# Performance work log

Measured on AMD Instinct MI355X. Metric: run time of the kernel, lower is better.

Reference implementation:

```python
import jax, jax.numpy as jnp
import numpy as np
from jax import lax

N_WIN = 232
T = 8            # timesteps
CHUNK = N_WIN // T  # 29
BETA = 0.9
THR = 1.0
POOL_DIV = 4.0 * 4.0 * 4.0  # avgpool3d kernel volume


@jax.custom_vjp
def spike(x):
    # Heaviside forward (snntorch fire: mem_shift > 0)
    return (x > 0).astype(x.dtype)

def _spike_fwd(x):
    return spike(x), x

def _spike_bwd(x, g):
    # snntorch ATan surrogate, alpha=2: grad = 1 / (1 + (pi*x)^2)
    return (g / (1.0 + (jnp.pi * x) ** 2),)

spike.defvjp(_spike_fwd, _spike_bwd)


def lif(cur, mem, beta, thr):
    # snntorch Leaky, reset_mechanism='subtract': reset uses previous mem
    reset = spike(mem - thr)
    mem_new = beta * mem + cur - reset * thr
    spk = spike(mem_new - thr)
    return spk, mem_new


def setup_inputs() -> dict:
    key = jax.random.key(0)
    ks = jax.random.split(key, 8)
    B, C, H, W = 16, 3, 96, 96
    h0, h1 = 2048, 1024
    input_dim = 47 * 47       # 2209
    in_feat = C * h1 * 13     # 39936
    return {
        "x": jax.random.normal(ks[0], (B, C, N_WIN, H, W), jnp.float32),
        "W_in": jax.random.normal(ks[1], (h0, input_dim), jnp.float32) / np.sqrt(input_dim).astype(np.float32),
        "b_in": jax.random.normal(ks[2], (h0,), jnp.float32) * 0.01,
        "W_hid": jax.random.normal(ks[3], (h1, h0), jnp.float32) / np.sqrt(h0).astype(np.float32),
        "b_hid": jax.random.normal(ks[4], (h1,), jnp.float32) * 0.01,
        "W_out": jax.random.normal(ks[5], (4, in_feat), jnp.float32) / np.sqrt(in_feat).astype(np.float32),
        "b_out": jax.random.normal(ks[6], (4,), jnp.float32) * 0.01,
    }


def reference(x, W_in, b_in, W_hid, b_hid, W_out, b_out):
    B, C, _, H, W = x.shape
    # split time into T chunks of CHUNK, pool each chunk independently
    x6 = x[:, :, : T * CHUNK].reshape(B, C, T, CHUNK, H, W)
    pooled = lax.reduce_window(x6, 0.0, lax.add,
                               (1, 1, 1, 4, 4, 4), (1, 1, 1, 2, 2, 2), "VALID") / POOL_DIV
    Dp, Hp, Wp = pooled.shape[3], pooled.shape[4], pooled.shape[5]  # 13, 47, 47
    # [T, B, C*Dp, Hp*Wp]
    xs = pooled.transpose(2, 0, 1, 3, 4, 5).reshape(T, B, C * Dp, Hp * Wp)
    # fc_in is per-step independent -> precompute for all steps
    cur_in_all = jnp.einsum("tbnf,hf->tbnh", xs, W_in) + b_in

    def step(carry, cur_in):
        m_in, m_hid, m_out = carry
        spk_in, m_in = lif(cur_in, m_in, BETA, THR)
        cur_hid = jnp.einsum("bnh,gh->bng", spk_in, W_hid) + b_hid
        spk_hid, m_hid = lif(cur_hid, m_hid, BETA, THR)
        cur_out = spk_hid.reshape(B, -1) @ W_out.T + b_out
        spk_out, m_out = lif(cur_out, m_out, BETA, 1.0)  # li_out threshold=1.0
        return (m_in, m_hid, m_out), spk_out

    init = (jnp.zeros((B, C * Dp, W_in.shape[0]), x.dtype),
            jnp.zeros((B, C * Dp, W_hid.shape[0]), x.dtype),
            jnp.zeros((B, W_out.shape[0]), x.dtype))
    _, spk_rec = lax.scan(step, init, cur_in_all)
    return spk_rec  # [T, B, n_classes]
```

## Files before the change

### kernel.cpp

```cpp
#include <hip/hip_runtime.h>
#include <hip/hip_bf16.h>

typedef unsigned short ushort_t;
typedef __bf16 bf16x8 __attribute__((ext_vector_type(8)));
typedef float f32x4 __attribute__((ext_vector_type(4)));

#define NROWS 4992
#define KPAD 2240
#define KREAL 2209
#define NH 2048

#define OFF_XS      ((size_t)0)
#define OFF_WINB    ((size_t)22364160)
#define OFF_CURIN   ((size_t)31539200)
#define OFF_CNT1    ((size_t)72433664)
#define OFF_BITS1   ((size_t)72453632)
#define OFF_CNT2    ((size_t)73731584)
#define OFF_BITS2   ((size_t)73732096)
#define ZERO_BYTES  ((size_t)(74371072 - 72433664))
#define OFF_LIST1   ((size_t)74371072)
#define OFF_LIST2   ((size_t)75649024)

__global__ __launch_bounds__(256) void convert_win(const float* __restrict__ W,
                                                   __hip_bfloat16* __restrict__ Wb) {
    int idx = blockIdx.x * 256 + threadIdx.x;
    int n = idx / KPAD, k = idx - n * KPAD;
    float v = (k < KREAL) ? W[(size_t)n * KREAL + k] : 0.f;
    Wb[idx] = __float2bfloat16(v);
}

__global__ __launch_bounds__(256) void pool_kernel(const float* __restrict__ x,
                                                   __hip_bfloat16* __restrict__ xs) {
    __shared__ float slice[9216];
    __shared__ float acc[2][2209];
    const int tid = threadIdx.x;
    const int blk = blockIdx.x;
    const int t = blk & 7;
    const int bc = blk >> 3;
    const int b = bc / 3, c = bc - b * 3;
    const float* xbase = x + ((size_t)bc * 232 + (size_t)t * 29) * 9216;

    for (int o = tid; o < 2209; o += 256) { acc[0][o] = 0.f; acc[1][o] = 0.f; }

    for (int z = 0; z < 28; ++z) {
        __syncthreads();
        const float4* src = (const float4*)(xbase + (size_t)z * 9216);
        float4* dst = (float4*)slice;
#pragma unroll
        for (int kk = 0; kk < 9; ++kk) dst[tid + kk * 256] = src[tid + kk * 256];
        __syncthreads();

        const int dmin = (z >= 3) ? ((z - 2) >> 1) : 0;
        int dmax = z >> 1; if (dmax > 12) dmax = 12;
        const bool emit = (z >= 3) && (z & 1);
        const int dem = (z - 3) >> 1;
        const int row = t * 624 + b * 39 + c * 13 + dem;

        for (int o = tid; o < 2209; o += 256) {
            int i = o / 47, j = o - i * 47;
            const float* p = slice + (2 * i) * 96 + 2 * j;
            float s = 0.f;
#pragma unroll
            for (int dy = 0; dy < 4; ++dy)
                s += p[dy * 96 + 0] + p[dy * 96 + 1] + p[dy * 96 + 2] + p[dy * 96 + 3];
            for (int d = dmin; d <= dmax; ++d) acc[d & 1][o] += s;
            if (emit) {
                int slot = dem & 1;
                xs[(size_t)row * KPAD + o] = __float2bfloat16(acc[slot][o] * 0.015625f);
                acc[slot][o] = 0.f;
            }
        }
        if (emit) {
            for (int o = KREAL + tid; o < KPAD; o += 256)
                xs[(size_t)row * KPAD + o] = __float2bfloat16(0.f);
        }
    }
}

__global__ __launch_bounds__(256) void gemm_kernel(const ushort_t* __restrict__ A,
                                                   const ushort_t* __restrict__ B,
                                                   float* __restrict__ C) {
    __shared__ ushort_t As[64 * 40];
    __shared__ ushort_t Bs[64 * 40];
    const int tid = threadIdx.x;
    const int m0 = blockIdx.y * 64, n0 = blockIdx.x * 64;
    const int lane = tid & 63, w = tid >> 6;
    const int wm = (w >> 1) * 32, wn = (w & 1) * 32;
    const int lr = lane & 15, quad = lane >> 4;

    f32x4 acc00 = {0.f,0.f,0.f,0.f}, acc01 = {0.f,0.f,0.f,0.f};
    f32x4 acc10 = {0.f,0.f,0.f,0.f}, acc11 = {0.f,0.f,0.f,0.f};

    const int r = tid >> 2, c8 = (tid & 3) * 8;
    const ushort_t* Ag = A + (size_t)(m0 + r) * KPAD + c8;
    const ushort_t* Bg = B + (size_t)(n0 + r) * KPAD + c8;
    ushort_t* Asw = &As[r * 40 + c8];
    ushort_t* Bsw = &Bs[r * 40 + c8];
    const ushort_t* Ar0 = &As[(wm + lr) * 40 + quad * 8];
    const ushort_t* Ar1 = &As[(wm + 16 + lr) * 40 + quad * 8];
    const ushort_t* Br0 = &Bs[(wn + lr) * 40 + quad * 8];
    const ushort_t* Br1 = &Bs[(wn + 16 + lr) * 40 + quad * 8];

    for (int k0 = 0; k0 < KPAD; k0 += 32) {
        __syncthreads();
        *(uint4*)Asw = *(const uint4*)(Ag + k0);
        *(uint4*)Bsw = *(const uint4*)(Bg + k0);
        __syncthreads();
        bf16x8 a0 = *(const bf16x8*)Ar0;
        bf16x8 a1 = *(const bf16x8*)Ar1;
        bf16x8 b0 = *(const bf16x8*)Br0;
        bf16x8 b1 = *(const bf16x8*)Br1;
        acc00 = __builtin_amdgcn_mfma_f32_16x16x32_bf16(a0, b0, acc00, 0, 0, 0);
        acc01 = __builtin_amdgcn_mfma_f32_16x16x32_bf16(a0, b1, acc01, 0, 0, 0);
        acc10 = __builtin_amdgcn_mfma_f32_16x16x32_bf16(a1, b0, acc10, 0, 0, 0);
        acc11 = __builtin_amdgcn_mfma_f32_16x16x32_bf16(a1, b1, acc11, 0, 0, 0);
    }
    const int colb = n0 + wn + lr;
    const int rowb = m0 + wm + quad * 4;
#pragma unroll
    for (int reg = 0; reg < 4; ++reg) {
        C[(size_t)(rowb + reg) * NH + colb]           = acc00[reg];
        C[(size_t)(rowb + reg) * NH + colb + 16]      = acc01[reg];
        C[(size_t)(rowb + 16 + reg) * NH + colb]      = acc10[reg];
        C[(size_t)(rowb + 16 + reg) * NH + colb + 16] = acc11[reg];
    }
}

__global__ __launch_bounds__(256) void lif1_kernel(const float* __restrict__ cur_in,
                                                   const float* __restrict__ b_in,
                                                   int* __restrict__ cnt1,
                                                   int* __restrict__ list1,
                                                   unsigned int* __restrict__ bits1) {
    const int h = blockIdx.x * 256 + threadIdx.x;
    const int row2 = blockIdx.y;
    const float bias = b_in[h];
    float m = 0.f;
#pragma unroll
    for (int t = 0; t < 8; ++t) {
        const int r = t * 624 + row2;
        float cur = cur_in[(size_t)r * NH + h] + bias;
        float reset = (m > 1.f) ? 1.f : 0.f;
        m = 0.9f * m + cur - reset;
        if (m > 1.f) {
            int idx = atomicAdd(&cnt1[r], 1);
            if (idx < 64) list1[r * 64 + idx] = h;
            atomicOr(&bits1[r * 64 + (h >> 5)], 1u << (h & 31));
        }
    }
}

__global__ __launch_bounds__(256) void lif2_kernel(const float* __restrict__ W_hid,
                                                   const float* __restrict__ b_hid,
                                                   const int* __restrict__ cnt1,
                                                   const int* __restrict__ list1,
                                                   const unsigned int* __restrict__ bits1,
                                                   int* __restrict__ cnt2,
                                                   int* __restrict__ list2,
                                                   unsigned int* __restrict__ bits2) {
    const int g = blockIdx.x * 256 + threadIdx.x;
    const int row2 = blockIdx.y;
    const int b = row2 / 39, n = row2 - b * 39;
    const float* Wg = W_hid + (size_t)g * NH;
    const float bias = b_hid[g];
    float m = 0.f;
    for (int t = 0; t < 8; ++t) {
        const int r = t * 624 + row2;
        float cur = bias;
        int c = cnt1[r];
        if (c > 0) {
            if (c <= 64) {
                for (int i2 = 0; i2 < c; ++i2) cur += Wg[list1[r * 64 + i2]];
            } else {
                for (int w2 = 0; w2 < 64; ++w2) {
                    unsigned int v = bits1[r * 64 + w2];
                    while (v) { int h = w2 * 32 + __ffs(v) - 1; v &= v - 1; cur += Wg[h]; }
                }
            }
        }
        float reset = (m > 1.f) ? 1.f : 0.f;
        m = 0.9f * m + cur - reset;
        if (m > 1.f) {
            int rb = t * 16 + b;
            int fidx = n * 1024 + g;
            int idx = atomicAdd(&cnt2[rb], 1);
            if (idx < 256) list2[rb * 256 + idx] = fidx;
            atomicOr(&bits2[rb * 1248 + (fidx >> 5)], 1u << (fidx & 31));
        }
    }
}

__global__ void lif3_kernel(const float* __restrict__ W_out,
                            const float* __restrict__ b_out,
                            const int* __restrict__ cnt2,
                            const int* __restrict__ list2,
                            const unsigned int* __restrict__ bits2,
                            float* __restrict__ out) {
    const int tid = threadIdx.x;
    const int b = tid >> 2, o = tid & 3;
    const float* Wo = W_out + (size_t)o * 39936;
    const float bias = b_out[o];
    float m = 0.f;
    for (int t = 0; t < 8; ++t) {
        const int rb = t * 16 + b;
        float cur = bias;
        int c = cnt2[rb];
        if (c > 0) {
            if (c <= 256) {
                for (int i2 = 0; i2 < c; ++i2) cur += Wo[list2[rb * 256 + i2]];
            } else {
                for (int w2 = 0; w2 < 1248; ++w2) {
                    unsigned int v = bits2[rb * 1248 + w2];
                    while (v) { int f = w2 * 32 + __ffs(v) - 1; v &= v - 1; cur += Wo[f]; }
                }
            }
        }
        float reset = (m > 1.f) ? 1.f : 0.f;
        m = 0.9f * m + cur - reset;
        out[t * 64 + b * 4 + o] = (m > 1.f) ? 1.f : 0.f;
    }
}

extern "C" void kernel_launch(void* const* d_in, const int* in_sizes, int n_in,
                              void* d_out, int out_size, void* d_ws, size_t ws_size,
                              hipStream_t stream) {
    const float* x     = (const float*)d_in[0];
    const float* W_in  = (const float*)d_in[1];
    const float* b_in  = (const float*)d_in[2];
    const float* W_hid = (const float*)d_in[3];
    const float* b_hid = (const float*)d_in[4];
    const float* W_out = (const float*)d_in[5];
    const float* b_out = (const float*)d_in[6];
    float* out = (float*)d_out;
    char* ws = (char*)d_ws;

    __hip_bfloat16* xs_bf  = (__hip_bfloat16*)(ws + OFF_XS);
    __hip_bfloat16* winb   = (__hip_bfloat16*)(ws + OFF_WINB);
    float*          cur_in = (float*)(ws + OFF_CURIN);
    int*            cnt1   = (int*)(ws + OFF_CNT1);
    unsigned int*   bits1  = (unsigned int*)(ws + OFF_BITS1);
    int*            cnt2   = (int*)(ws + OFF_CNT2);
    unsigned int*   bits2  = (unsigned int*)(ws + OFF_BITS2);
    int*            list1  = (int*)(ws + OFF_LIST1);
    int*            list2  = (int*)(ws + OFF_LIST2);

    hipMemsetAsync(ws + OFF_CNT1, 0, ZERO_BYTES, stream);

    convert_win<<<(2048 * KPAD) / 256, 256, 0, stream>>>(W_in, winb);
    pool_kernel<<<384, 256, 0, stream>>>(x, xs_bf);
    gemm_kernel<<<dim3(2048 / 64, NROWS / 64), 256, 0, stream>>>(
        (const ushort_t*)xs_bf, (const ushort_t*)winb, cur_in);
    lif1_kernel<<<dim3(8, 624), 256, 0, stream>>>(cur_in, b_in, cnt1, list1, bits1);
    lif2_kernel<<<dim3(4, 624), 256, 0, stream>>>(W_hid, b_hid, cnt1, list1, bits1,
                                                  cnt2, list2, bits2);
    lif3_kernel<<<1, 64, 0, stream>>>(W_out, b_out, cnt2, list2, bits2, out);
}
```

Measured before the change: 704.1 us.

## Split pooling into row bands and enlarge GEMM tiles with direct-to-LDS loads

The pooling kernel is split into four spatial row bands per (batch, channel, timestep) block. This quadruples the grid and shrinks shared memory, which should raise occupancy on the bandwidth-bound input read. The fc_in GEMM moves from 64x64 to 128x128 block tiles with a 4x4 MFMA grid per wave, which gives more operand reuse per LDS load. It also fills shared memory with global_load_lds and drops the register staging. The unpadded 32-element LDS rows may cause bank conflicts on fragment reads, and the larger accumulator array raises register pressure.

```diff
diff --git a/kernel.cpp b/kernel.cpp
--- a/kernel.cpp
+++ b/kernel.cpp
@@ -21,6 +21,10 @@
 #define OFF_LIST1   ((size_t)74371072)
 #define OFF_LIST2   ((size_t)75649024)
 
+#define GLOAD16(g, l) __builtin_amdgcn_global_load_lds( \
+    (const __attribute__((address_space(1))) void*)(g), \
+    (__attribute__((address_space(3))) void*)(l), 16, 0, 0)
+
 __global__ __launch_bounds__(256) void convert_win(const float* __restrict__ W,
                                                    __hip_bfloat16* __restrict__ Wb) {
     int idx = blockIdx.x * 256 + threadIdx.x;
@@ -31,23 +35,27 @@
 
 __global__ __launch_bounds__(256) void pool_kernel(const float* __restrict__ x,
                                                    __hip_bfloat16* __restrict__ xs) {
-    __shared__ float slice[9216];
-    __shared__ float acc[2][2209];
+    __shared__ float slice[26 * 96];
+    __shared__ float acc[2][12 * 47];
     const int tid = threadIdx.x;
+    const int band = blockIdx.y;
     const int blk = blockIdx.x;
     const int t = blk & 7;
     const int bc = blk >> 3;
     const int b = bc / 3, c = bc - b * 3;
-    const float* xbase = x + ((size_t)bc * 232 + (size_t)t * 29) * 9216;
-
-    for (int o = tid; o < 2209; o += 256) { acc[0][o] = 0.f; acc[1][o] = 0.f; }
+    const int i0 = band * 12;
+    const int ni = (band == 3) ? 11 : 12;
+    const int nyf4 = (2 * ni + 2) * 24;
+    const int nout = ni * 47;
+    const float* xbase = x + ((size_t)bc * 232 + (size_t)t * 29) * 9216 + i0 * 192;
+
+    for (int o = tid; o < nout; o += 256) { acc[0][o] = 0.f; acc[1][o] = 0.f; }
 
     for (int z = 0; z < 28; ++z) {
         __syncthreads();
         const float4* src = (const float4*)(xbase + (size_t)z * 9216);
         float4* dst = (float4*)slice;
-#pragma unroll
-        for (int kk = 0; kk < 9; ++kk) dst[tid + kk * 256] = src[tid + kk * 256];
+        for (int idx = tid; idx < nyf4; idx += 256) dst[idx] = src[idx];
         __syncthreads();
 
         const int dmin = (z >= 3) ? ((z - 2) >> 1) : 0;
@@ -56,9 +64,9 @@
         const int dem = (z - 3) >> 1;
         const int row = t * 624 + b * 39 + c * 13 + dem;
 
-        for (int o = tid; o < 2209; o += 256) {
-            int i = o / 47, j = o - i * 47;
-            const float* p = slice + (2 * i) * 96 + 2 * j;
+        for (int o = tid; o < nout; o += 256) {
+            int il = o / 47, j = o - il * 47;
+            const float* p = slice + (2 * il) * 96 + 2 * j;
             float s = 0.f;
 #pragma unroll
             for (int dy = 0; dy < 4; ++dy)
@@ -66,63 +74,73 @@
             for (int d = dmin; d <= dmax; ++d) acc[d & 1][o] += s;
             if (emit) {
                 int slot = dem & 1;
-                xs[(size_t)row * KPAD + o] = __float2bfloat16(acc[slot][o] * 0.015625f);
+                xs[(size_t)row * KPAD + i0 * 47 + o] = __float2bfloat16(acc[slot][o] * 0.015625f);
                 acc[slot][o] = 0.f;
             }
         }
-        if (emit) {
-            for (int o = KREAL + tid; o < KPAD; o += 256)
-                xs[(size_t)row * KPAD + o] = __float2bfloat16(0.f);
-        }
-    }
-}
-
+        if (emit && band == 0 && tid < KPAD - KREAL) {
+            xs[(size_t)row * KPAD + KREAL + tid] = __float2bfloat16(0.f);
+        }
+    }
+}
+
+#define BM 128
+#define BN 128
+#define BK 32
 __global__ __launch_bounds__(256) void gemm_kernel(const ushort_t* __restrict__ A,
                                                    const ushort_t* __restrict__ B,
                                                    float* __restrict__ C) {
-    __shared__ ushort_t As[64 * 40];
-    __shared__ ushort_t Bs[64 * 40];
+    __shared__ ushort_t As[BM * BK];
+    __shared__ ushort_t Bs[BN * BK];
     const int tid = threadIdx.x;
-    const int m0 = blockIdx.y * 64, n0 = blockIdx.x * 64;
+    const int m0 = blockIdx.y * BM, n0 = blockIdx.x * BN;
     const int lane = tid & 63, w = tid >> 6;
-    const int wm = (w >> 1) * 32, wn = (w & 1) * 32;
+    const int wm = (w >> 1) * 64, wn = (w & 1) * 64;
     const int lr = lane & 15, quad = lane >> 4;
 
-    f32x4 acc00 = {0.f,0.f,0.f,0.f}, acc01 = {0.f,0.f,0.f,0.f};
-    f32x4 acc10 = {0.f,0.f,0.f,0.f}, acc11 = {0.f,0.f,0.f,0.f};
-
-    const int r = tid >> 2, c8 = (tid & 3) * 8;
-    const ushort_t* Ag = A + (size_t)(m0 + r) * KPAD + c8;
-    const ushort_t* Bg = B + (size_t)(n0 + r) * KPAD + c8;
-    ushort_t* Asw = &As[r * 40 + c8];
-    ushort_t* Bsw = &Bs[r * 40 + c8];
-    const ushort_t* Ar0 = &As[(wm + lr) * 40 + quad * 8];
-    const ushort_t* Ar1 = &As[(wm + 16 + lr) * 40 + quad * 8];
-    const ushort_t* Br0 = &Bs[(wn + lr) * 40 + quad * 8];
-    const ushort_t* Br1 = &Bs[(wn + 16 + lr) * 40 + quad * 8];
-
-    for (int k0 = 0; k0 < KPAD; k0 += 32) {
-        __syncthreads();
-        *(uint4*)Asw = *(const uint4*)(Ag + k0);
-        *(uint4*)Bsw = *(const uint4*)(Bg + k0);
-        __syncthreads();
-        bf16x8 a0 = *(const bf16x8*)Ar0;
-        bf16x8 a1 = *(const bf16x8*)Ar1;
-        bf16x8 b0 = *(const bf16x8*)Br0;
-        bf16x8 b1 = *(const bf16x8*)Br1;
-        acc00 = __builtin_amdgcn_mfma_f32_16x16x32_bf16(a0, b0, acc00, 0, 0, 0);
-        acc01 = __builtin_amdgcn_mfma_f32_16x16x32_bf16(a0, b1, acc01, 0, 0, 0);
-        acc10 = __builtin_amdgcn_mfma_f32_16x16x32_bf16(a1, b0, acc10, 0, 0, 0);
-        acc11 = __builtin_amdgcn_mfma_f32_16x16x32_bf16(a1, b1, acc11, 0, 0, 0);
-    }
-    const int colb = n0 + wn + lr;
-    const int rowb = m0 + wm + quad * 4;
-#pragma unroll
-    for (int reg = 0; reg < 4; ++reg) {
-        C[(size_t)(rowb + reg) * NH + colb]           = acc00[reg];
-        C[(size_t)(rowb + reg) * NH + colb + 16]      = acc01[reg];
-        C[(size_t)(rowb + 16 + reg) * NH + colb]      = acc10[reg];
-        C[(size_t)(rowb + 16 + reg) * NH + colb + 16] = acc11[reg];
+    f32x4 acc[4][4] = {};
+
+    const int srow = tid >> 2;
+    const int sk = (tid & 3) * 8;
+    const ushort_t* Ag0 = A + (size_t)(m0 + srow) * KPAD + sk;
+    const ushort_t* Ag1 = A + (size_t)(m0 + 64 + srow) * KPAD + sk;
+    const ushort_t* Bg0 = B + (size_t)(n0 + srow) * KPAD + sk;
+    const ushort_t* Bg1 = B + (size_t)(n0 + 64 + srow) * KPAD + sk;
+    ushort_t* Asl0 = &As[srow * BK + sk];
+    ushort_t* Asl1 = &As[(64 + srow) * BK + sk];
+    ushort_t* Bsl0 = &Bs[srow * BK + sk];
+    ushort_t* Bsl1 = &Bs[(64 + srow) * BK + sk];
+
+    for (int k0 = 0; k0 < KPAD; k0 += BK) {
+        __syncthreads();
+        GLOAD16(Ag0 + k0, Asl0);
+        GLOAD16(Ag1 + k0, Asl1);
+        GLOAD16(Bg0 + k0, Bsl0);
+        GLOAD16(Bg1 + k0, Bsl1);
+        __syncthreads();
+        bf16x8 af[4], bfr[4];
+#pragma unroll
+        for (int i = 0; i < 4; ++i)
+            af[i] = *(const bf16x8*)&As[(wm + i * 16 + lr) * BK + quad * 8];
+#pragma unroll
+        for (int j = 0; j < 4; ++j)
+            bfr[j] = *(const bf16x8*)&Bs[(wn + j * 16 + lr) * BK + quad * 8];
+#pragma unroll
+        for (int i = 0; i < 4; ++i)
+#pragma unroll
+            for (int j = 0; j < 4; ++j)
+                acc[i][j] = __builtin_amdgcn_mfma_f32_16x16x32_bf16(af[i], bfr[j], acc[i][j], 0, 0, 0);
+    }
+#pragma unroll
+    for (int i = 0; i < 4; ++i) {
+        const int row = m0 + wm + i * 16 + quad * 4;
+#pragma unroll
+        for (int j = 0; j < 4; ++j) {
+            const int col = n0 + wn + j * 16 + lr;
+#pragma unroll
+            for (int reg = 0; reg < 4; ++reg)
+                C[(size_t)(row + reg) * NH + col] = acc[i][j][reg];
+        }
     }
 }
 
@@ -246,8 +264,8 @@
     hipMemsetAsync(ws + OFF_CNT1, 0, ZERO_BYTES, stream);
 
     convert_win<<<(2048 * KPAD) / 256, 256, 0, stream>>>(W_in, winb);
-    pool_kernel<<<384, 256, 0, stream>>>(x, xs_bf);
-    gemm_kernel<<<dim3(2048 / 64, NROWS / 64), 256, 0, stream>>>(
+    pool_kernel<<<dim3(384, 4), 256, 0, stream>>>(x, xs_bf);
+    gemm_kernel<<<dim3(NH / BN, NROWS / BM), 256, 0, stream>>>(
         (const ushort_t*)xs_bf, (const ushort_t*)winb, cur_in);
     lif1_kernel<<<dim3(8, 624), 256, 0, stream>>>(cur_in, b_in, cnt1, list1, bits1);
     lif2_kernel<<<dim3(4, 624), 256, 0, stream>>>(W_hid, b_hid, cnt1, list1, bits1,
```

Measured after the change: 700.9 us. About the same (-0.4%).
